# Performance work log

Measured on AMD Instinct MI355X. Metric: run time of the kernel, lower is better.

## Reference

```python
import jax, jax.numpy as jnp
import numpy as np

N = 100000  # num_nodes


def setup_inputs() -> dict:
    key = jax.random.key(0)
    k1, k2, k3, k4 = jax.random.split(key, 4)
    nodes = jax.random.randint(k1, (10000,), 0, N)
    edge_index = jax.random.randint(k2, (2, 1600000), 0, N)
    emb_weight = jax.random.normal(k3, (N, 512), dtype=jnp.float32)
    W = jax.random.normal(k4, (512, 128), dtype=jnp.float32) * 0.05
    return {"nodes": nodes, "edge_index": edge_index, "emb_weight": emb_weight, "W": W}


def reference(nodes, edge_index, emb_weight, W):
    # GCNConv (PyG semantics, bias=False): add self-loops, symmetric deg
    # normalization, linear transform, scatter-add aggregation into targets.
    num_nodes = emb_weight.shape[0]
    loops = jnp.arange(num_nodes, dtype=edge_index.dtype)
    row = jnp.concatenate([edge_index[0], loops])  # sources (x_j)
    col = jnp.concatenate([edge_index[1], loops])  # targets (aggregation)

    ones = jnp.ones(row.shape[0], dtype=emb_weight.dtype)
    deg = jax.ops.segment_sum(ones, col, num_segments=num_nodes)
    dinv = jnp.where(deg > 0, jax.lax.rsqrt(deg), 0.0)
    norm = dinv[row] * dinv[col]  # [E+N]

    h = emb_weight @ W  # [N, C] dense transform (main GEMM)
    msg = h[row] * norm[:, None]  # gather + scale, [E+N, C]
    out = jax.ops.segment_sum(msg, col, num_segments=num_nodes)  # scatter-add
    return out[nodes]
```

## Files before the change

kernel.cpp:

```cpp
#include <hip/hip_runtime.h>
#include <hip/hip_bf16.h>


constexpr int KDIM = 512;
constexpr int CDIM = 128;
constexpr int CAPB = 64;
constexpr int CAPO = 16;

typedef __attribute__((ext_vector_type(8))) short short8;
typedef __attribute__((ext_vector_type(4))) float f32x4;

static __device__ __forceinline__ unsigned short f2bf(float f) {
    unsigned u = __float_as_uint(f);
    unsigned r = ((u >> 16) & 1u) + 0x7fffu;
    return (unsigned short)((u + r) >> 16);
}
static __device__ __forceinline__ float bf2f(unsigned short b) {
    return __uint_as_float(((unsigned)b) << 16);
}

__global__ void k_init(int* __restrict__ deg, int* __restrict__ tmap,
                       int* __restrict__ cur, int* __restrict__ ocnt,
                       int* __restrict__ ucount, int N, int n) {
    int i = blockIdx.x * blockDim.x + threadIdx.x;
    if (i < N) { deg[i] = 0; tmap[i] = -1; }
    if (i < n) { cur[i] = 0; ocnt[i] = 0; }
    if (i == 0) *ucount = 0;
}

__global__ void k_targets(const int* __restrict__ nodes, int n,
                          int* __restrict__ tmap, int* __restrict__ tlist,
                          int* __restrict__ ucount) {
    int i = blockIdx.x * blockDim.x + threadIdx.x;
    if (i >= n) return;
    int v = nodes[i];
    if (atomicCAS(&tmap[v], -1, -2) == -1) {
        int slot = atomicAdd(ucount, 1);
        tlist[slot] = v;
        tmap[v] = slot;
    }
}

__global__ void k_prep(const float* __restrict__ W, unsigned short* __restrict__ wt,
                       const int* __restrict__ nodes, int n,
                       const int* __restrict__ tmap,
                       int* __restrict__ ocnt, int* __restrict__ olist) {
    if (blockIdx.x < 256) {
        int idx = blockIdx.x * 256 + threadIdx.x;
        int j  = idx & 7;
        int l  = (idx >> 3) & 63;
        int st = idx >> 9;
        int t  = st & 7, s = st >> 3;
        int k  = s * 32 + (l >> 4) * 8 + j;
        int c  = t * 16 + (l & 15);
        wt[idx] = f2bf(W[(size_t)k * CDIM + c]);
    } else {
        int i = (blockIdx.x - 256) * 256 + threadIdx.x;
        if (i >= n) return;
        int slot = tmap[nodes[i]];
        int p = atomicAdd(&ocnt[slot], 1);
        if (p < CAPO) olist[slot * CAPO + p] = i;
    }
}

__global__ __launch_bounds__(256)
void k_degfill(const int* __restrict__ erow, const int* __restrict__ ecol, int E,
               int* __restrict__ deg, const int* __restrict__ tmap,
               int* __restrict__ cur, int* __restrict__ ebuf) {
    int t = blockIdx.x * blockDim.x + threadIdx.x;
    int base = t * 4;
    if (base >= E) return;
    if (base + 4 <= E) {
        int4 c = *reinterpret_cast<const int4*>(ecol + base);
        atomicAdd(&deg[c.x], 1);
        atomicAdd(&deg[c.y], 1);
        atomicAdd(&deg[c.z], 1);
        atomicAdd(&deg[c.w], 1);
        int s0 = tmap[c.x], s1 = tmap[c.y], s2 = tmap[c.z], s3 = tmap[c.w];
        if ((s0 >= 0) | (s1 >= 0) | (s2 >= 0) | (s3 >= 0)) {
            int4 r = *reinterpret_cast<const int4*>(erow + base);
            if (s0 >= 0) { int p = atomicAdd(&cur[s0], 1); if (p < CAPB) ebuf[s0 * CAPB + p] = r.x; }
            if (s1 >= 0) { int p = atomicAdd(&cur[s1], 1); if (p < CAPB) ebuf[s1 * CAPB + p] = r.y; }
            if (s2 >= 0) { int p = atomicAdd(&cur[s2], 1); if (p < CAPB) ebuf[s2 * CAPB + p] = r.z; }
            if (s3 >= 0) { int p = atomicAdd(&cur[s3], 1); if (p < CAPB) ebuf[s3 * CAPB + p] = r.w; }
        }
    } else {
        for (int i = base; i < E; ++i) {
            int c = ecol[i];
            atomicAdd(&deg[c], 1);
            int s = tmap[c];
            if (s >= 0) { int p = atomicAdd(&cur[s], 1); if (p < CAPB) ebuf[s * CAPB + p] = erow[i]; }
        }
    }
}

__global__ __launch_bounds__(512, 2)
void k_gemm_h(const float* __restrict__ emb, const unsigned short* __restrict__ wt,
              unsigned short* __restrict__ h, int N) {
    extern __shared__ char smem[];
    float*          sA = (float*)smem;
    unsigned short* sB = (unsigned short*)(smem + 3 * 16384);
    int tid  = threadIdx.x;
    int lane = tid & 63;
    int wid  = tid >> 6;
    int wr   = wid >> 1;
    int wc   = wid & 1;
    int row0 = blockIdx.x * 128;

    auto stage = [&](int buf, int kc) {
        #pragma unroll
        for (int p = 0; p < 2; ++p) {
            int i = p * 512 + tid;
            int row = i >> 3, chunk = i & 7;
            int swz = chunk ^ (row & 7);
            int rg = row0 + row; if (rg >= N) rg = N - 1;
            const float* g = emb + (size_t)rg * KDIM + kc * 32 + swz * 4;
            float* l = sA + buf * 4096 + i * 4;
            __builtin_amdgcn_global_load_lds(
                (const __attribute__((address_space(1))) void*)g,
                (__attribute__((address_space(3))) void*)l, 16, 0, 0);
        }
        {
            const unsigned short* g = wt + (size_t)kc * 4096 + tid * 8;
            unsigned short* l = sB + buf * 4096 + tid * 8;
            __builtin_amdgcn_global_load_lds(
                (const __attribute__((address_space(1))) void*)g,
                (__attribute__((address_space(3))) void*)l, 16, 0, 0);
        }
    };

    f32x4 acc[2][4];
    #pragma unroll
    for (int m = 0; m < 2; ++m)
        #pragma unroll
        for (int t = 0; t < 4; ++t) acc[m][t] = (f32x4){0.f, 0.f, 0.f, 0.f};

    int arow0 = wr * 32 + (lane & 15);
    int kq    = lane >> 4;

    auto compute = [&](int buf) {
        const float*          Ab = sA + buf * 4096;
        const unsigned short* Bb = sB + buf * 4096;
        short8 af[2];
        #pragma unroll
        for (int m = 0; m < 2; ++m) {
            int row = arow0 + m * 16;
            int c0  = kq * 2;
            int s0  = c0 ^ (row & 7);
            int s1  = (c0 + 1) ^ (row & 7);
            float4 v0 = *reinterpret_cast<const float4*>(Ab + row * 32 + s0 * 4);
            float4 v1 = *reinterpret_cast<const float4*>(Ab + row * 32 + s1 * 4);
            af[m][0] = (short)f2bf(v0.x); af[m][1] = (short)f2bf(v0.y);
            af[m][2] = (short)f2bf(v0.z); af[m][3] = (short)f2bf(v0.w);
            af[m][4] = (short)f2bf(v1.x); af[m][5] = (short)f2bf(v1.y);
            af[m][6] = (short)f2bf(v1.z); af[m][7] = (short)f2bf(v1.w);
        }
        #pragma unroll
        for (int tt = 0; tt < 4; ++tt) {
            int t = wc * 4 + tt;
            short8 bf = *reinterpret_cast<const short8*>(Bb + ((size_t)(t * 64 + lane)) * 8);
            acc[0][tt] = __builtin_amdgcn_mfma_f32_16x16x32_bf16(af[0], bf, acc[0][tt], 0, 0, 0);
            acc[1][tt] = __builtin_amdgcn_mfma_f32_16x16x32_bf16(af[1], bf, acc[1][tt], 0, 0, 0);
        }
    };

    stage(0, 0); stage(1, 1); stage(2, 2);

    for (int kc = 0; kc < 14; ++kc) {
        if (kc > 0) stage((kc + 2) % 3, kc + 2);
        asm volatile("s_waitcnt vmcnt(6)" ::: "memory");
        __builtin_amdgcn_s_barrier();
        asm volatile("" ::: "memory");
        compute(kc % 3);
        asm volatile("" ::: "memory");
        __builtin_amdgcn_s_barrier();
    }
    asm volatile("s_waitcnt vmcnt(3)" ::: "memory");
    __builtin_amdgcn_s_barrier();
    asm volatile("" ::: "memory");
    compute(2);
    asm volatile("" ::: "memory");
    __builtin_amdgcn_s_barrier();
    asm volatile("s_waitcnt vmcnt(0)" ::: "memory");
    __builtin_amdgcn_s_barrier();
    asm volatile("" ::: "memory");
    compute(0);

    __syncthreads();
    unsigned short* sC = (unsigned short*)smem;
    int rl0 = wr * 32 + (lane >> 4) * 4;
    int cl0 = wc * 64 + (lane & 15);
    #pragma unroll
    for (int m = 0; m < 2; ++m)
        #pragma unroll
        for (int tt = 0; tt < 4; ++tt)
            #pragma unroll
            for (int j = 0; j < 4; ++j)
                sC[(rl0 + m * 16 + j) * 128 + cl0 + tt * 16] = f2bf(acc[m][tt][j]);
    __syncthreads();
    #pragma unroll
    for (int c = 0; c < 4; ++c) {
        int i = c * 512 + tid;
        int row = i >> 4, off = i & 15;
        int r = row0 + row;
        if (r < N)
            *reinterpret_cast<short8*>(h + (size_t)r * CDIM + off * 8) =
                *reinterpret_cast<const short8*>(sC + row * 128 + off * 8);
    }
}

__global__ __launch_bounds__(256)
void k_agg(const unsigned short* __restrict__ h, const int* __restrict__ deg,
           const int* __restrict__ tlist, const int* __restrict__ cur,
           const int* __restrict__ ebuf, const int* __restrict__ ucount,
           const int* __restrict__ ocnt, const int* __restrict__ olist,
           float* __restrict__ out) {
    int u = *ucount;
    int slot = blockIdx.x * 4 + (threadIdx.x >> 6);
    if (slot >= u) return;
    int lane = threadIdx.x & 63;
    int e = min(cur[slot], CAPB);
    int myi = 0; float myw = 0.f;
    if (lane < e) {
        myi = ebuf[(size_t)slot * CAPB + lane];
        myw = rsqrtf((float)(deg[myi] + 1));
    }
    float ax = 0.f, ay = 0.f;
    #pragma unroll 4
    for (int j = 0; j < e; ++j) {
        int   src = __shfl(myi, j, 64);
        float w   = __shfl(myw, j, 64);
        unsigned v = *reinterpret_cast<const unsigned*>(h + (size_t)src * CDIM + lane * 2);
        ax += w * bf2f((unsigned short)(v & 0xffffu));
        ay += w * bf2f((unsigned short)(v >> 16));
    }
    int t = tlist[slot];
    float dt = rsqrtf((float)(deg[t] + 1));
    unsigned v = *reinterpret_cast<const unsigned*>(h + (size_t)t * CDIM + lane * 2);
    float rx = dt * (ax + dt * bf2f((unsigned short)(v & 0xffffu)));
    float ry = dt * (ay + dt * bf2f((unsigned short)(v >> 16)));
    int cnt = min(ocnt[slot], CAPO);
    for (int q = 0; q < cnt; ++q) {
        int i = olist[slot * CAPO + q];
        float2 o; o.x = rx; o.y = ry;
        *reinterpret_cast<float2*>(out + (size_t)i * CDIM + lane * 2) = o;
    }
}

extern "C" void kernel_launch(void* const* d_in, const int* in_sizes, int n_in,
                              void* d_out, int out_size, void* d_ws, size_t ws_size,
                              hipStream_t stream) {
    const int*   nodes = (const int*)d_in[0];
    const int*   eidx  = (const int*)d_in[1];
    const float* emb   = (const float*)d_in[2];
    const float* W     = (const float*)d_in[3];
    float*       out   = (float*)d_out;

    int n = in_sizes[0];
    int E = in_sizes[1] / 2;
    int N = in_sizes[2] / KDIM;
    const int* erow = eidx;
    const int* ecol = eidx + E;

    char* ws = (char*)d_ws;
    size_t o = 0;
    auto carve = [&](size_t bytes) {
        char* p = ws + o;
        o = (o + bytes + 255) & ~(size_t)255;
        return p;
    };
    int* deg    = (int*)carve((size_t)N * 4);
    int* tmap   = (int*)carve((size_t)N * 4);
    int* tlist  = (int*)carve((size_t)n * 4);
    int* cur    = (int*)carve((size_t)n * 4);
    int* ocnt   = (int*)carve((size_t)n * 4);
    int* olist  = (int*)carve((size_t)n * CAPO * 4);
    int* ucount = (int*)carve(4);
    int* ebuf   = (int*)carve((size_t)n * CAPB * 4);
    unsigned short* wt = (unsigned short*)carve((size_t)16 * 8 * 64 * 8 * 2);
    unsigned short* h  = (unsigned short*)carve((size_t)N * CDIM * 2);
    (void)ws_size; (void)n_in; (void)out_size;

    hipFuncSetAttribute(reinterpret_cast<const void*>(k_gemm_h),
                        hipFuncAttributeMaxDynamicSharedMemorySize, 73728);

    int E4 = (E + 3) / 4;
    k_init   <<<(N + 255) / 256, 256, 0, stream>>>(deg, tmap, cur, ocnt, ucount, N, n);
    k_targets<<<(n + 255) / 256, 256, 0, stream>>>(nodes, n, tmap, tlist, ucount);
    k_prep   <<<256 + (n + 255) / 256, 256, 0, stream>>>(W, wt, nodes, n, tmap, ocnt, olist);
    k_degfill<<<(E4 + 255) / 256, 256, 0, stream>>>(erow, ecol, E, deg, tmap, cur, ebuf);
    k_gemm_h <<<(N + 127) / 128, 512, 73728, stream>>>(emb, wt, h, N);
    k_agg    <<<(n + 3) / 4, 256, 0, stream>>>(h, deg, tlist, cur, ebuf, ucount,
                                               ocnt, olist, out);
}
```

Before: 156.4 us.

## Fuse GEMM, degree/edge-fill and output-list kernels into one launch

Merges the weight-conversion work into the init kernel. The GEMM, degree counting/edge bucketing and output-list building become one kernel whose block index picks the role. The goal is to remove launch gaps and let the atomic-heavy edge pass overlap with the memory-bound GEMM. The trade-off is that non-GEMM blocks now reserve the GEMM's large shared memory allocation and 512-thread shape, which can hurt their occupancy.

```diff
diff --git a/kernel.cpp b/kernel.cpp
--- a/kernel.cpp
+++ b/kernel.cpp
@@ -21,11 +21,22 @@
 
 __global__ void k_init(int* __restrict__ deg, int* __restrict__ tmap,
                        int* __restrict__ cur, int* __restrict__ ocnt,
-                       int* __restrict__ ucount, int N, int n) {
+                       int* __restrict__ ucount,
+                       const float* __restrict__ W, unsigned short* __restrict__ wt,
+                       int N, int n) {
     int i = blockIdx.x * blockDim.x + threadIdx.x;
     if (i < N) { deg[i] = 0; tmap[i] = -1; }
     if (i < n) { cur[i] = 0; ocnt[i] = 0; }
     if (i == 0) *ucount = 0;
+    if (i < 65536) {
+        int j  = i & 7;
+        int l  = (i >> 3) & 63;
+        int st = i >> 9;
+        int t  = st & 7, s = st >> 3;
+        int k  = s * 32 + (l >> 4) * 8 + j;
+        int c  = t * 16 + (l & 15);
+        wt[i] = f2bf(W[(size_t)k * CDIM + c]);
+    }
 }
 
 __global__ void k_targets(const int* __restrict__ nodes, int n,
@@ -41,62 +52,52 @@
     }
 }
 
-__global__ void k_prep(const float* __restrict__ W, unsigned short* __restrict__ wt,
-                       const int* __restrict__ nodes, int n,
-                       const int* __restrict__ tmap,
-                       int* __restrict__ ocnt, int* __restrict__ olist) {
-    if (blockIdx.x < 256) {
-        int idx = blockIdx.x * 256 + threadIdx.x;
-        int j  = idx & 7;
-        int l  = (idx >> 3) & 63;
-        int st = idx >> 9;
-        int t  = st & 7, s = st >> 3;
-        int k  = s * 32 + (l >> 4) * 8 + j;
-        int c  = t * 16 + (l & 15);
-        wt[idx] = f2bf(W[(size_t)k * CDIM + c]);
-    } else {
-        int i = (blockIdx.x - 256) * 256 + threadIdx.x;
+__global__ __launch_bounds__(512, 2)
+void k_main(const float* __restrict__ emb, const unsigned short* __restrict__ wt,
+            unsigned short* __restrict__ h, int N,
+            const int* __restrict__ erow, const int* __restrict__ ecol, int E,
+            int* __restrict__ deg, const int* __restrict__ tmap,
+            int* __restrict__ cur, int* __restrict__ ebuf,
+            const int* __restrict__ nodes, int n,
+            int* __restrict__ ocnt, int* __restrict__ olist,
+            int GB, int DB) {
+    int bid = (int)blockIdx.x;
+    if (bid >= GB + DB) {
+        int i = (bid - GB - DB) * 512 + threadIdx.x;
         if (i >= n) return;
         int slot = tmap[nodes[i]];
         int p = atomicAdd(&ocnt[slot], 1);
         if (p < CAPO) olist[slot * CAPO + p] = i;
-    }
-}
-
-__global__ __launch_bounds__(256)
-void k_degfill(const int* __restrict__ erow, const int* __restrict__ ecol, int E,
-               int* __restrict__ deg, const int* __restrict__ tmap,
-               int* __restrict__ cur, int* __restrict__ ebuf) {
-    int t = blockIdx.x * blockDim.x + threadIdx.x;
-    int base = t * 4;
-    if (base >= E) return;
-    if (base + 4 <= E) {
-        int4 c = *reinterpret_cast<const int4*>(ecol + base);
-        atomicAdd(&deg[c.x], 1);
-        atomicAdd(&deg[c.y], 1);
-        atomicAdd(&deg[c.z], 1);
-        atomicAdd(&deg[c.w], 1);
-        int s0 = tmap[c.x], s1 = tmap[c.y], s2 = tmap[c.z], s3 = tmap[c.w];
-        if ((s0 >= 0) | (s1 >= 0) | (s2 >= 0) | (s3 >= 0)) {
-            int4 r = *reinterpret_cast<const int4*>(erow + base);
-            if (s0 >= 0) { int p = atomicAdd(&cur[s0], 1); if (p < CAPB) ebuf[s0 * CAPB + p] = r.x; }
-            if (s1 >= 0) { int p = atomicAdd(&cur[s1], 1); if (p < CAPB) ebuf[s1 * CAPB + p] = r.y; }
-            if (s2 >= 0) { int p = atomicAdd(&cur[s2], 1); if (p < CAPB) ebuf[s2 * CAPB + p] = r.z; }
-            if (s3 >= 0) { int p = atomicAdd(&cur[s3], 1); if (p < CAPB) ebuf[s3 * CAPB + p] = r.w; }
-        }
-    } else {
-        for (int i = base; i < E; ++i) {
-            int c = ecol[i];
-            atomicAdd(&deg[c], 1);
-            int s = tmap[c];
-            if (s >= 0) { int p = atomicAdd(&cur[s], 1); if (p < CAPB) ebuf[s * CAPB + p] = erow[i]; }
-        }
-    }
-}
-
-__global__ __launch_bounds__(512, 2)
-void k_gemm_h(const float* __restrict__ emb, const unsigned short* __restrict__ wt,
-              unsigned short* __restrict__ h, int N) {
+        return;
+    }
+    if (bid >= GB) {
+        int t = (bid - GB) * 512 + threadIdx.x;
+        int base = t * 4;
+        if (base >= E) return;
+        if (base + 4 <= E) {
+            int4 c = *reinterpret_cast<const int4*>(ecol + base);
+            atomicAdd(&deg[c.x], 1);
+            atomicAdd(&deg[c.y], 1);
+            atomicAdd(&deg[c.z], 1);
+            atomicAdd(&deg[c.w], 1);
+            int s0 = tmap[c.x], s1 = tmap[c.y], s2 = tmap[c.z], s3 = tmap[c.w];
+            if ((s0 >= 0) | (s1 >= 0) | (s2 >= 0) | (s3 >= 0)) {
+                int4 r = *reinterpret_cast<const int4*>(erow + base);
+                if (s0 >= 0) { int p = atomicAdd(&cur[s0], 1); if (p < CAPB) ebuf[s0 * CAPB + p] = r.x; }
+                if (s1 >= 0) { int p = atomicAdd(&cur[s1], 1); if (p < CAPB) ebuf[s1 * CAPB + p] = r.y; }
+                if (s2 >= 0) { int p = atomicAdd(&cur[s2], 1); if (p < CAPB) ebuf[s2 * CAPB + p] = r.z; }
+                if (s3 >= 0) { int p = atomicAdd(&cur[s3], 1); if (p < CAPB) ebuf[s3 * CAPB + p] = r.w; }
+            }
+        } else {
+            for (int i = base; i < E; ++i) {
+                int c = ecol[i];
+                atomicAdd(&deg[c], 1);
+                int s = tmap[c];
+                if (s >= 0) { int p = atomicAdd(&cur[s], 1); if (p < CAPB) ebuf[s * CAPB + p] = erow[i]; }
+            }
+        }
+        return;
+    }
     extern __shared__ char smem[];
     float*          sA = (float*)smem;
     unsigned short* sB = (unsigned short*)(smem + 3 * 16384);
@@ -105,7 +106,7 @@
     int wid  = tid >> 6;
     int wr   = wid >> 1;
     int wc   = wid & 1;
-    int row0 = blockIdx.x * 128;
+    int row0 = bid * 128;
 
     auto stage = [&](int buf, int kc) {
         #pragma unroll
@@ -281,15 +282,17 @@
     unsigned short* h  = (unsigned short*)carve((size_t)N * CDIM * 2);
     (void)ws_size; (void)n_in; (void)out_size;
 
-    hipFuncSetAttribute(reinterpret_cast<const void*>(k_gemm_h),
+    hipFuncSetAttribute(reinterpret_cast<const void*>(k_main),
                         hipFuncAttributeMaxDynamicSharedMemorySize, 73728);
 
-    int E4 = (E + 3) / 4;
-    k_init   <<<(N + 255) / 256, 256, 0, stream>>>(deg, tmap, cur, ocnt, ucount, N, n);
+    int GB = (N + 127) / 128;
+    int DB = (E + 2047) / 2048;
+    int OB = (n + 511) / 512;
+    k_init   <<<(N + 255) / 256, 256, 0, stream>>>(deg, tmap, cur, ocnt, ucount, W, wt, N, n);
     k_targets<<<(n + 255) / 256, 256, 0, stream>>>(nodes, n, tmap, tlist, ucount);
-    k_prep   <<<256 + (n + 255) / 256, 256, 0, stream>>>(W, wt, nodes, n, tmap, ocnt, olist);
-    k_degfill<<<(E4 + 255) / 256, 256, 0, stream>>>(erow, ecol, E, deg, tmap, cur, ebuf);
-    k_gemm_h <<<(N + 127) / 128, 512, 73728, stream>>>(emb, wt, h, N);
+    k_main   <<<GB + DB + OB, 512, 73728, stream>>>(emb, wt, h, N,
+                                                    erow, ecol, E, deg, tmap, cur, ebuf,
+                                                    nodes, n, ocnt, olist, GB, DB);
     k_agg    <<<(n + 3) / 4, 256, 0, stream>>>(h, deg, tlist, cur, ebuf, ucount,
                                                ocnt, olist, out);
 }
```

Measured after the change: 138.1 us. 1.13x faster.
